# Kernel tuning notes

Hardware: AMD Instinct MI355X
Metric: run time of the kernel (lower is better)

The kernel has to match this reference:

```python
import jax, jax.numpy as jnp
import numpy as np

B, S, D = 32, 1024, 1024   # batch, seq_len, d_model
P, F = 4, 4096             # num_phases, d_ff
# Each phase owns a contiguous split of S/P sequence positions (set_splits builds
# a disjoint contiguous partition of the sequence; assert t == seq_length).


def setup_inputs() -> dict:
    key = jax.random.key(0)
    ks = jax.random.split(key, 6)
    x = jax.random.normal(ks[0], (B, S, D), dtype=jnp.float32)
    phases = jax.random.randint(ks[1], (B, S), 0, P, dtype=jnp.int32)
    s1 = 1.0 / np.sqrt(D)
    s2 = 1.0 / np.sqrt(F)
    W1 = jax.random.uniform(ks[2], (P, D, F), jnp.float32, -s1, s1)
    b1 = jax.random.uniform(ks[3], (P, F), jnp.float32, -s1, s1)
    W2 = jax.random.uniform(ks[4], (P, F, D), jnp.float32, -s2, s2)
    b2 = jax.random.uniform(ks[5], (P, D), jnp.float32, -s2, s2)
    return {"x": x, "W1": W1, "b1": b1, "W2": W2, "b2": b2, "phases": phases}


def reference(x, W1, b1, W2, b2, phases):
    # Branched path (phases.ndim > 1): gather each phase's contiguous split,
    # run that phase's FF, scatter back. Since the static phase_mask is a
    # contiguous equal partition, gather/scatter == reshape into [B, P, S/P, D].
    xs = x.reshape(B, P, S // P, D)
    h = jax.nn.relu(jnp.einsum('bpsd,pdf->bpsf', xs, W1) + b1[None, :, None, :])
    y = jnp.einsum('bpsf,pfd->bpsd', h, W2) + b2[None, :, None, :]
    return y.reshape(B, S, D)
```

## Files before the change

### kernel.cpp

```cpp
#include <hip/hip_runtime.h>
#include <hip/hip_bf16.h>
#include <stdint.h>

typedef __bf16 bf16_t;
typedef bf16_t bf16x8 __attribute__((ext_vector_type(8)));
typedef bf16_t bf16x4 __attribute__((ext_vector_type(4)));
typedef float  f32x4  __attribute__((ext_vector_type(4)));

#define AS1(p) ((const __attribute__((address_space(1))) void*)(p))
#define AS3(p) ((__attribute__((address_space(3))) void*)(p))

static constexpr int B_ = 32, S_ = 1024, D_ = 1024, P_ = 4, F_ = 4096;
static constexpr int SPP = S_ / P_;
static constexpr int MP  = B_ * SPP;

__global__ void conv_x_kernel(const float* __restrict__ x, bf16_t* __restrict__ xg) {
  const int64_t n4 = (int64_t)B_ * S_ * D_ / 4;
  for (int64_t i = (int64_t)blockIdx.x * blockDim.x + threadIdx.x; i < n4;
       i += (int64_t)gridDim.x * blockDim.x) {
    int64_t e = i << 2;
    int d = (int)(e & (D_ - 1));
    int s = (int)((e >> 10) & (S_ - 1));
    int b = (int)(e >> 20);
    int p = s >> 8;
    int r = (b << 8) | (s & 255);
    const float4 v = ((const float4*)x)[i];
    bf16x4 o;
    o[0] = (bf16_t)v.x; o[1] = (bf16_t)v.y; o[2] = (bf16_t)v.z; o[3] = (bf16_t)v.w;
    *(bf16x4*)&xg[(((int64_t)p * MP + r) << 10) | d] = o;
  }
}

__global__ void conv_wt_kernel(const float* __restrict__ W, bf16_t* __restrict__ Wt,
                               int K, int N) {
  __shared__ bf16_t tile[32][33];
  const int p = blockIdx.z;
  const float* Wp = W + (int64_t)p * K * N;
  bf16_t* Wtp = Wt + (int64_t)p * K * N;
  const int n0 = blockIdx.x * 32, k0 = blockIdx.y * 32;
  const int tx = threadIdx.x & 31, ty = threadIdx.x >> 5;
  #pragma unroll
  for (int j = 0; j < 4; ++j) {
    int kr = ty + j * 8;
    tile[kr][tx] = (bf16_t)Wp[(int64_t)(k0 + kr) * N + n0 + tx];
  }
  __syncthreads();
  #pragma unroll
  for (int j = 0; j < 4; ++j) {
    int nr = ty + j * 8;
    Wtp[(int64_t)(n0 + nr) * K + k0 + tx] = tile[tx][nr];
  }
}


__device__ __forceinline__ bf16x8 ldsfrag(const char* region, int row, int cb) {
  return *(const bf16x8*)(region + row * 128 + (cb ^ ((row & 7) << 4)));
}

template<int LDK>
__device__ __forceinline__ void stage_half(const bf16_t* gsrc, char* ldsreg, int t) {
  #pragma unroll
  for (int j = 0; j < 2; ++j) {
    const int idx = j * 512 + t;
    const int row = idx >> 3;
    const int cb  = ((idx & 7) << 4) ^ ((row & 7) << 4);
    __builtin_amdgcn_global_load_lds(AS1((const char*)(gsrc + (int64_t)row * LDK) + cb),
                                     AS3(ldsreg + idx * 16), 16, 0, 0);
  }
}

#define MFMA_QUAD(AF, BF, MO, NO) \
  do { _Pragma("unroll") for (int m_ = 0; m_ < 4; ++m_) \
       _Pragma("unroll") for (int n_ = 0; n_ < 2; ++n_) \
       _Pragma("unroll") for (int k_ = 0; k_ < 2; ++k_) \
         acc[(MO) + m_][(NO) + n_] = __builtin_amdgcn_mfma_f32_16x16x32_bf16( \
             AF[m_][k_], BF[n_][k_], acc[(MO) + m_][(NO) + n_], 0, 0, 0); } while (0)

#define FRAG_A(DST, BUF, MO) \
  do { _Pragma("unroll") for (int m_ = 0; m_ < 4; ++m_) { \
         DST[m_][0] = *(const bf16x8*)(baseA_k0 + (BUF) * 32768 + ((MO) + m_) * 2048); \
         DST[m_][1] = *(const bf16x8*)(baseA_k1 + (BUF) * 32768 + ((MO) + m_) * 2048); } } while (0)

#define FRAG_B(DST, BUF, NO) \
  do { _Pragma("unroll") for (int n_ = 0; n_ < 2; ++n_) { \
         DST[n_][0] = *(const bf16x8*)(baseB_k0 + (BUF) * 32768 + ((NO) + n_) * 2048); \
         DST[n_][1] = *(const bf16x8*)(baseB_k1 + (BUF) * 32768 + ((NO) + n_) * 2048); } } while (0)

#define BAR()   __builtin_amdgcn_s_barrier()
#define SBAR()  __builtin_amdgcn_sched_barrier(0)
#define PRIO(x) __builtin_amdgcn_s_setprio(x)
#define VMCNT6() asm volatile("s_waitcnt vmcnt(6)" ::: "memory")
#define VMCNT0() asm volatile("s_waitcnt vmcnt(0)" ::: "memory")

template<bool RELU, bool OUT_BF16, int KK, int NN>
__global__ __launch_bounds__(512, 2)
void ffgemm8_kernel(const bf16_t* __restrict__ A, const bf16_t* __restrict__ Bt,
                    const float* __restrict__ bias, void* __restrict__ outv, int M) {
  static_assert(KK % 128 == 0, "need even number of 64-wide K tiles");
  __shared__ __align__(16) char smem[131072];
  char* const At0 = smem;
  char* const At1 = smem + 32768;
  char* const Bs0 = smem + 65536;
  char* const Bs1 = smem + 98304;

  const int t = threadIdx.x, lane = t & 63, w = t >> 6;
  const int wm = w >> 2, wn = w & 3;
  const int fr = lane & 15, hi = lane >> 4;

  const int xorm = (fr & 7) << 4;
  const char* const baseA_k0 = At0 + (wm * 128 + fr) * 128 + ((hi * 16) ^ xorm);
  const char* const baseA_k1 = At0 + (wm * 128 + fr) * 128 + ((64 + hi * 16) ^ xorm);
  const char* const baseB_k0 = Bs0 + (wn * 64 + fr) * 128 + ((hi * 16) ^ xorm);
  const char* const baseB_k1 = Bs0 + (wn * 64 + fr) * 128 + ((64 + hi * 16) ^ xorm);

  const int gx = gridDim.x, gy = gridDim.y;
  const int nwg = gx * gy * (int)gridDim.z;
  const int id  = ((int)blockIdx.z * gy + (int)blockIdx.y) * gx + (int)blockIdx.x;
  const int swz = (id & 7) * (nwg >> 3) + (id >> 3);
  const int per_p = gx * gy;
  const int p  = swz / per_p;
  const int q  = swz % per_p;
  const int band = q / (gx * 4), qq = q % (gx * 4);
  const int bx = qq >> 2, by = band * 4 + (qq & 3);

  const int tile_m = by * 256, tile_n = bx * 256;
  const bf16_t* Ab = A  + (int64_t)p * M  * KK + (int64_t)tile_m * KK;
  const bf16_t* Bb = Bt + (int64_t)p * NN * KK + (int64_t)tile_n * KK;
  const float* biasp = bias + (int64_t)p * NN;

  f32x4 acc[8][4] = {};
  constexpr int NI = KK / 128;

  stage_half<KK>(Ab,                          At0,          t);
  stage_half<KK>(Ab + (int64_t)128 * KK,      At0 + 16384,  t);
  stage_half<KK>(Bb,                          Bs0,          t);
  stage_half<KK>(Bb + (int64_t)128 * KK,      Bs0 + 16384,  t);
  stage_half<KK>(Bb + 64,                     Bs1,          t);
  stage_half<KK>(Bb + (int64_t)128 * KK + 64, Bs1 + 16384,  t);
  stage_half<KK>(Ab + 64,                     At1,          t);
  VMCNT6();
  BAR(); SBAR();

  for (int i = 0; i < NI; ++i) {
    const int k0 = i * 128;
    const bool more = (i < NI - 1);
    bf16x8 a0[4][2], a1[4][2], b0[2][2], b1[2][2];

    FRAG_A(a0, 0, 0); FRAG_B(b0, 0, 0);
    PRIO(1); MFMA_QUAD(a0, b0, 0, 0); PRIO(0);
    FRAG_B(b1, 0, 2);
    stage_half<KK>(Ab + (int64_t)128 * KK + (k0 + 64), At1 + 16384, t);
    SBAR(); BAR();
    PRIO(1); MFMA_QUAD(a0, b1, 0, 2); PRIO(0);
    FRAG_A(a1, 0, 4);
    SBAR(); BAR();
    PRIO(1); MFMA_QUAD(a1, b0, 4, 0); PRIO(0);
    if (more) { stage_half<KK>(Bb + (k0 + 128), Bs0, t);
                stage_half<KK>(Bb + (int64_t)128 * KK + (k0 + 128), Bs0 + 16384, t); }
    SBAR(); BAR();
    PRIO(1); MFMA_QUAD(a1, b1, 4, 2); PRIO(0);
    if (more) stage_half<KK>(Ab + (k0 + 128), At0, t);
    if (more) VMCNT6(); else VMCNT0();
    SBAR(); BAR();

    FRAG_A(a0, 1, 0); FRAG_B(b0, 1, 0);
    PRIO(1); MFMA_QUAD(a0, b0, 0, 0); PRIO(0);
    FRAG_B(b1, 1, 2);
    if (more) stage_half<KK>(Ab + (int64_t)128 * KK + (k0 + 128), At0 + 16384, t);
    SBAR(); BAR();
    PRIO(1); MFMA_QUAD(a0, b1, 0, 2); PRIO(0);
    FRAG_A(a1, 1, 4);
    SBAR(); BAR();
    PRIO(1); MFMA_QUAD(a1, b0, 4, 0); PRIO(0);
    if (more) { stage_half<KK>(Bb + (k0 + 192), Bs1, t);
                stage_half<KK>(Bb + (int64_t)128 * KK + (k0 + 192), Bs1 + 16384, t); }
    SBAR(); BAR();
    PRIO(1); MFMA_QUAD(a1, b1, 4, 2); PRIO(0);
    if (more) stage_half<KK>(Ab + (k0 + 192), At1, t);
    if (more) VMCNT6(); else VMCNT0();
    SBAR(); BAR();
  }

  float bv[4];
  #pragma unroll
  for (int n = 0; n < 4; ++n) bv[n] = biasp[tile_n + wn * 64 + n * 16 + fr];
  if (OUT_BF16) {
    bf16_t* out = (bf16_t*)outv + (int64_t)p * M * NN;
    #pragma unroll
    for (int m = 0; m < 8; ++m)
      #pragma unroll
      for (int j = 0; j < 4; ++j) {
        const int row = tile_m + wm * 128 + m * 16 + hi * 4 + j;
        #pragma unroll
        for (int n = 0; n < 4; ++n) {
          const int col = tile_n + wn * 64 + n * 16 + fr;
          float v = acc[m][n][j] + bv[n];
          if (RELU) v = fmaxf(v, 0.0f);
          out[(int64_t)row * NN + col] = (bf16_t)v;
        }
      }
  } else {
    float* out = (float*)outv;
    #pragma unroll
    for (int m = 0; m < 8; ++m)
      #pragma unroll
      for (int j = 0; j < 4; ++j) {
        const int row = tile_m + wm * 128 + m * 16 + hi * 4 + j;
        const int grow = ((row >> 8) << 10) + p * SPP + (row & 255);
        #pragma unroll
        for (int n = 0; n < 4; ++n) {
          const int col = tile_n + wn * 64 + n * 16 + fr;
          out[(int64_t)grow * NN + col] = acc[m][n][j] + bv[n];
        }
      }
  }
}

extern "C" void kernel_launch(void* const* d_in, const int* in_sizes, int n_in,
                              void* d_out, int out_size, void* d_ws, size_t ws_size,
                              hipStream_t stream) {
  (void)in_sizes; (void)n_in; (void)out_size; (void)ws_size;
  const float* x  = (const float*)d_in[0];
  const float* W1 = (const float*)d_in[1];
  const float* b1 = (const float*)d_in[2];
  const float* W2 = (const float*)d_in[3];
  const float* b2 = (const float*)d_in[4];
  float* y = (float*)d_out;

  char* ws = (char*)d_ws;
  bf16_t* xg = (bf16_t*)ws;
  bf16_t* wt = (bf16_t*)(ws + (size_t)64 * 1024 * 1024);
  bf16_t* h  = (bf16_t*)(ws + (size_t)96 * 1024 * 1024);

  conv_x_kernel<<<2048, 256, 0, stream>>>(x, xg);
  conv_wt_kernel<<<dim3(F_ / 32, D_ / 32, P_), 256, 0, stream>>>(W1, wt, D_, F_);
  ffgemm8_kernel<true, true, 1024, 4096><<<dim3(F_ / 256, MP / 256, P_), 512, 0, stream>>>(
      xg, wt, b1, h, MP);
  conv_wt_kernel<<<dim3(D_ / 32, F_ / 32, P_), 256, 0, stream>>>(W2, wt, F_, D_);
  ffgemm8_kernel<false, false, 4096, 1024><<<dim3(D_ / 256, MP / 256, P_), 512, 0, stream>>>(
      h, wt, b2, y, MP);
}
```

Measured before the change: 560.6 us.

## Replace staggered 8-phase LDS pipeline with simpler two-stage double buffering

The fine-grained eight-phase schedule is replaced. It interleaved half-tile global-to-LDS loads with four barriers per K-tile and partial vmcnt(6) waits. The new loop is a plain double-buffer ping-pong: all fragments for one buffer are read into registers, the full next K-tile is issued into the other buffer, and the MFMAs run with one vmcnt(0) and one barrier per half-iteration. The MFMA loop order now puts k outermost, so consecutive MFMAs target different accumulators. This cuts barrier count, but full vmcnt(0) waits may expose more memory latency than the staggered scheme did.

```diff
diff --git a/kernel.cpp b/kernel.cpp
--- a/kernel.cpp
+++ b/kernel.cpp
@@ -70,9 +70,9 @@
 }
 
 #define MFMA_QUAD(AF, BF, MO, NO) \
-  do { _Pragma("unroll") for (int m_ = 0; m_ < 4; ++m_) \
+  do { _Pragma("unroll") for (int k_ = 0; k_ < 2; ++k_) \
+       _Pragma("unroll") for (int m_ = 0; m_ < 4; ++m_) \
        _Pragma("unroll") for (int n_ = 0; n_ < 2; ++n_) \
-       _Pragma("unroll") for (int k_ = 0; k_ < 2; ++k_) \
          acc[(MO) + m_][(NO) + n_] = __builtin_amdgcn_mfma_f32_16x16x32_bf16( \
              AF[m_][k_], BF[n_][k_], acc[(MO) + m_][(NO) + n_], 0, 0, 0); } while (0)
 
@@ -89,7 +89,6 @@
 #define BAR()   __builtin_amdgcn_s_barrier()
 #define SBAR()  __builtin_amdgcn_sched_barrier(0)
 #define PRIO(x) __builtin_amdgcn_s_setprio(x)
-#define VMCNT6() asm volatile("s_waitcnt vmcnt(6)" ::: "memory")
 #define VMCNT0() asm volatile("s_waitcnt vmcnt(0)" ::: "memory")
 
 template<bool RELU, bool OUT_BF16, int KK, int NN>
@@ -129,55 +128,46 @@
   const float* biasp = bias + (int64_t)p * NN;
 
   f32x4 acc[8][4] = {};
-  constexpr int NI = KK / 128;
-
-  stage_half<KK>(Ab,                          At0,          t);
-  stage_half<KK>(Ab + (int64_t)128 * KK,      At0 + 16384,  t);
-  stage_half<KK>(Bb,                          Bs0,          t);
-  stage_half<KK>(Bb + (int64_t)128 * KK,      Bs0 + 16384,  t);
-  stage_half<KK>(Bb + 64,                     Bs1,          t);
-  stage_half<KK>(Bb + (int64_t)128 * KK + 64, Bs1 + 16384,  t);
-  stage_half<KK>(Ab + 64,                     At1,          t);
-  VMCNT6();
+  constexpr int NI2 = KK / 128;
+
+  stage_half<KK>(Ab,                       At0,          t);
+  stage_half<KK>(Ab + (int64_t)128 * KK,   At0 + 16384,  t);
+  stage_half<KK>(Bb,                       Bs0,          t);
+  stage_half<KK>(Bb + (int64_t)128 * KK,   Bs0 + 16384,  t);
+  VMCNT0();
   BAR(); SBAR();
 
-  for (int i = 0; i < NI; ++i) {
-    const int k0 = i * 128;
-    const bool more = (i < NI - 1);
+  for (int j = 0; j < NI2; ++j) {
+    const int kX = j * 128;
+    const bool more = (j < NI2 - 1);
     bf16x8 a0[4][2], a1[4][2], b0[2][2], b1[2][2];
 
-    FRAG_A(a0, 0, 0); FRAG_B(b0, 0, 0);
-    PRIO(1); MFMA_QUAD(a0, b0, 0, 0); PRIO(0);
-    FRAG_B(b1, 0, 2);
-    stage_half<KK>(Ab + (int64_t)128 * KK + (k0 + 64), At1 + 16384, t);
+    FRAG_A(a0, 0, 0); FRAG_B(b0, 0, 0); FRAG_B(b1, 0, 2);
+    stage_half<KK>(Ab + (kX + 64),                      At1,          t);
+    stage_half<KK>(Ab + (int64_t)128 * KK + (kX + 64),  At1 + 16384,  t);
+    stage_half<KK>(Bb + (kX + 64),                      Bs1,          t);
+    stage_half<KK>(Bb + (int64_t)128 * KK + (kX + 64),  Bs1 + 16384,  t);
+    PRIO(1); MFMA_QUAD(a0, b0, 0, 0); PRIO(0); SBAR();
+    FRAG_A(a1, 0, 4);
+    PRIO(1); MFMA_QUAD(a0, b1, 0, 2); PRIO(0); SBAR();
+    PRIO(1); MFMA_QUAD(a1, b0, 4, 0); PRIO(0); SBAR();
+    PRIO(1); MFMA_QUAD(a1, b1, 4, 2); PRIO(0);
+    VMCNT0();
     SBAR(); BAR();
-    PRIO(1); MFMA_QUAD(a0, b1, 0, 2); PRIO(0);
-    FRAG_A(a1, 0, 4);
-    SBAR(); BAR();
-    PRIO(1); MFMA_QUAD(a1, b0, 4, 0); PRIO(0);
-    if (more) { stage_half<KK>(Bb + (k0 + 128), Bs0, t);
-                stage_half<KK>(Bb + (int64_t)128 * KK + (k0 + 128), Bs0 + 16384, t); }
-    SBAR(); BAR();
+
+    FRAG_A(a0, 1, 0); FRAG_B(b0, 1, 0); FRAG_B(b1, 1, 2);
+    if (more) {
+      stage_half<KK>(Ab + (kX + 128),                     At0,          t);
+      stage_half<KK>(Ab + (int64_t)128 * KK + (kX + 128), At0 + 16384,  t);
+      stage_half<KK>(Bb + (kX + 128),                     Bs0,          t);
+      stage_half<KK>(Bb + (int64_t)128 * KK + (kX + 128), Bs0 + 16384,  t);
+    }
+    PRIO(1); MFMA_QUAD(a0, b0, 0, 0); PRIO(0); SBAR();
+    FRAG_A(a1, 1, 4);
+    PRIO(1); MFMA_QUAD(a0, b1, 0, 2); PRIO(0); SBAR();
+    PRIO(1); MFMA_QUAD(a1, b0, 4, 0); PRIO(0); SBAR();
     PRIO(1); MFMA_QUAD(a1, b1, 4, 2); PRIO(0);
-    if (more) stage_half<KK>(Ab + (k0 + 128), At0, t);
-    if (more) VMCNT6(); else VMCNT0();
-    SBAR(); BAR();
-
-    FRAG_A(a0, 1, 0); FRAG_B(b0, 1, 0);
-    PRIO(1); MFMA_QUAD(a0, b0, 0, 0); PRIO(0);
-    FRAG_B(b1, 1, 2);
-    if (more) stage_half<KK>(Ab + (int64_t)128 * KK + (k0 + 128), At0 + 16384, t);
-    SBAR(); BAR();
-    PRIO(1); MFMA_QUAD(a0, b1, 0, 2); PRIO(0);
-    FRAG_A(a1, 1, 4);
-    SBAR(); BAR();
-    PRIO(1); MFMA_QUAD(a1, b0, 4, 0); PRIO(0);
-    if (more) { stage_half<KK>(Bb + (k0 + 192), Bs1, t);
-                stage_half<KK>(Bb + (int64_t)128 * KK + (k0 + 192), Bs1 + 16384, t); }
-    SBAR(); BAR();
-    PRIO(1); MFMA_QUAD(a1, b1, 4, 2); PRIO(0);
-    if (more) stage_half<KK>(Ab + (k0 + 192), At1, t);
-    if (more) VMCNT6(); else VMCNT0();
+    if (more) VMCNT0();
     SBAR(); BAR();
   }
 
@@ -189,12 +179,12 @@
     #pragma unroll
     for (int m = 0; m < 8; ++m)
       #pragma unroll
-      for (int j = 0; j < 4; ++j) {
-        const int row = tile_m + wm * 128 + m * 16 + hi * 4 + j;
+      for (int j2 = 0; j2 < 4; ++j2) {
+        const int row = tile_m + wm * 128 + m * 16 + hi * 4 + j2;
         #pragma unroll
         for (int n = 0; n < 4; ++n) {
           const int col = tile_n + wn * 64 + n * 16 + fr;
-          float v = acc[m][n][j] + bv[n];
+          float v = acc[m][n][j2] + bv[n];
           if (RELU) v = fmaxf(v, 0.0f);
           out[(int64_t)row * NN + col] = (bf16_t)v;
         }
@@ -204,13 +194,13 @@
     #pragma unroll
     for (int m = 0; m < 8; ++m)
       #pragma unroll
-      for (int j = 0; j < 4; ++j) {
-        const int row = tile_m + wm * 128 + m * 16 + hi * 4 + j;
+      for (int j2 = 0; j2 < 4; ++j2) {
+        const int row = tile_m + wm * 128 + m * 16 + hi * 4 + j2;
         const int grow = ((row >> 8) << 10) + p * SPP + (row & 255);
         #pragma unroll
         for (int n = 0; n < 4; ++n) {
           const int col = tile_n + wn * 64 + n * 16 + fr;
-          out[(int64_t)grow * NN + col] = acc[m][n][j] + bv[n];
+          out[(int64_t)grow * NN + col] = acc[m][n][j2] + bv[n];
         }
       }
   }
```

Measured after the change: 610.6 us. +8.9%, slower.
